# Kernel optimization log

Measured on AMD Instinct MI355X. Metric: run time of the kernel, lower is better.

The kernel has to match this reference:

```python
import jax, jax.numpy as jnp
import numpy as np


def _skip_plan(T, skip_size):
    """Static per-step plan replicating Python list indexing h_i_skips[i - skip_size].

    Returns (slots, use_zero): slot k means 'use h from k+1 steps ago' in the
    rolling buffer (buf[0] == h_{i-1}); use_zero==1 means the skip input is a
    zero init vector.
    """
    slots = np.zeros(T, np.int32)
    use_zero = np.zeros(T, np.float32)
    for i in range(T):
        if i < skip_size:
            # negative Python index: element 2*i of [skip_size zeros] + appended h's
            if 2 * i < skip_size:
                use_zero[i] = 1.0
            else:
                # h_j with j = 2*i - skip_size  ->  lag = i - j = skip_size - i
                slots[i] = (skip_size - i) - 1
        else:
            if i - skip_size < skip_size:
                use_zero[i] = 1.0  # one of the zero inits
            else:
                slots[i] = 2 * skip_size - 1  # h_{i - 2*skip_size}
    return jnp.asarray(slots), jnp.asarray(use_zero)


def setup_inputs() -> dict:
    key = jax.random.key(0)
    ks = jax.random.split(key, 7)
    B, T, X, H = 64, 512, 256, 1024
    s = 1.0 / float(np.sqrt(H))  # PyTorch GRUCell init scale
    x = jax.random.normal(ks[0], (B, T, X), jnp.float32)
    W_ih = jax.random.uniform(ks[1], (3 * H, X), jnp.float32, -s, s)
    W_hh = jax.random.uniform(ks[2], (3 * H, H), jnp.float32, -s, s)
    b_ih = jax.random.uniform(ks[3], (3 * H,), jnp.float32, -s, s)
    b_hh = jax.random.uniform(ks[4], (3 * H,), jnp.float32, -s, s)
    w1 = jax.random.randint(ks[5], (T,), 0, 2, jnp.int32)
    w2_rand = jax.random.randint(ks[6], (T,), 0, 2, jnp.int32)
    w2 = jnp.where(w1 == 0, 1, w2_rand)  # original: W_2 = 1 if W_1 == 0
    return {"x": x, "W_ih": W_ih, "W_hh": W_hh, "b_ih": b_ih, "b_hh": b_hh,
            "w1": w1, "w2": w2, "skip_size": 5}


def reference(x, W_ih, W_hh, b_ih, b_hh, w1, w2, skip_size):
    B, T, X = x.shape
    H = W_hh.shape[1]
    slots, use_zero = _skip_plan(T, int(skip_size))
    # Batch all input projections up-front: [T, B, 3H]
    xi = jnp.einsum('btx,gx->tbg', x, W_ih) + b_ih
    L = 2 * int(skip_size)
    buf0 = jnp.zeros((L, B, H), x.dtype)  # buf[k] = h_{i-1-k}
    w1f = w1.astype(x.dtype)
    w2f = w2.astype(x.dtype)

    def step(buf, xs):
        xi_t, a, b, slot, uz = xs
        h_orig = buf[0]
        h_skip = jax.lax.dynamic_index_in_dim(buf, slot, 0, keepdims=False)
        h = h_orig * a + h_skip * b * (1.0 - uz)
        hh = h @ W_hh.T + b_hh
        xr, xz, xn = jnp.split(xi_t, 3, axis=-1)
        hr, hz, hn = jnp.split(hh, 3, axis=-1)
        r = jax.nn.sigmoid(xr + hr)
        z = jax.nn.sigmoid(xz + hz)
        n = jnp.tanh(xn + r * hn)
        h_new = (1.0 - z) * n + z * h
        buf = jnp.concatenate([h_new[None], buf[:-1]], axis=0)
        return buf, None

    buf, _ = jax.lax.scan(step, buf0, (xi, w1f, w2f, slots, use_zero))
    # h_i_original + h_i_skip, and chunk(repeat) makes them identical
    return 2.0 * buf[0]
```

## Files before the change

kernel.cpp:

```cpp
#include <hip/hip_runtime.h>
#include <hip/hip_bf16.h>
#include <type_traits>

typedef short bf16x8 __attribute__((ext_vector_type(8)));
typedef short bf16x4 __attribute__((ext_vector_type(4)));
typedef float f32x4  __attribute__((ext_vector_type(4)));
typedef int   i32x4  __attribute__((ext_vector_type(4)));
typedef unsigned long long u64;

#define B_   64
#define T_   512
#define XD_  256
#define H_   1024
#define NWG  256
#define NTH  512

#define OFF_WCAT  0UL
#define SZ_WCAT   (3072UL*1280*2)
#define OFF_XB    (OFF_WCAT + SZ_WCAT)
#define SZ_XB     ((unsigned long)T_*B_*XD_*2)
#define OFF_HBF16 (OFF_XB + SZ_XB)
#define SZ_HBF16  (2UL*B_*H_*2)
#define OFF_PLAN  (OFF_HBF16 + SZ_HBF16)
#define SZ_PLAN   (4096UL)
#define OFF_CNT   (OFF_PLAN + SZ_PLAN)
#define SZ_CNT    (8192UL)

__device__ __forceinline__ float sigm_(float x) { return 1.f / (1.f + __expf(-x)); }
__device__ __forceinline__ float tanh_(float x) { return 1.f - 2.f / (__expf(2.f * x) + 1.f); }
__device__ __forceinline__ short bf16_of(float f) {
    __hip_bfloat16 h = __float2bfloat16(f);
    return *reinterpret_cast<short*>(&h);
}
__device__ __forceinline__ float f_of_bf16(short s) {
    union { unsigned u; float f; } c;
    c.u = ((unsigned)(unsigned short)s) << 16;
    return c.f;
}

__global__ void prep_wcat(const float* __restrict__ W_ih, const float* __restrict__ W_hh,
                          short* __restrict__ Wcat) {
    const int j = blockIdx.x;
    for (int k = threadIdx.x; k < 1280; k += 256) {
        float v = (k < XD_) ? W_ih[j * XD_ + k] : W_hh[j * H_ + (k - XD_)];
        Wcat[(long)j * 1280 + k] = bf16_of(v);
    }
}

__global__ void prep_xb(const float* __restrict__ x, short* __restrict__ xb) {
    const long total = (long)T_ * B_ * XD_;
    for (long i = (long)blockIdx.x * blockDim.x + threadIdx.x; i < total;
         i += (long)gridDim.x * blockDim.x) {
        int t   = (int)(i >> 14);
        int rem = (int)(i & 16383);
        int b   = rem >> 8;
        int k   = rem & 255;
        xb[i] = bf16_of(x[((long)(b * T_ + t)) * XD_ + k]);
    }
}

__global__ void prep_plan(const int* __restrict__ w1, const int* __restrict__ w2,
                          const int* __restrict__ ssp, int* __restrict__ plang) {
    int t = threadIdx.x;
    if (t > T_) return;
    if (t == T_) { plang[t] = (1 << 2); return; }
    int ss = ssp[0];
    int a = w1[t] & 1;
    int uz = 0, slot = 0;
    if (t < ss)            { if (2 * t < ss) uz = 1; else slot = ss - t - 1; }
    else if (t - ss < ss)  { uz = 1; }
    else                   { slot = 2 * ss - 1; }
    int bet = uz ? 0 : (w2[t] & 1);
    plang[t] = a | (bet << 1) | ((slot + 1) << 2);
}

__global__ void prep_zero(short* __restrict__ hbf16, int* __restrict__ cnt) {
    int i = blockIdx.x * blockDim.x + threadIdx.x;
    if (i < B_ * H_) hbf16[i] = 0;
    if (i < (int)(SZ_CNT / 4)) cnt[i] = 0;
}

__global__ __launch_bounds__(NTH, 1) void persist_kernel(
    const short* __restrict__ Wcat, const short* __restrict__ xb,
    const float* __restrict__ b_ih, const float* __restrict__ b_hh,
    short* __restrict__ hbf16, const int* __restrict__ plang,
    int* __restrict__ cnt, float* __restrict__ out) {

    __shared__ short Wlds[48 * 1280];
    __shared__ float red[3][7][64][4];
    __shared__ short ringl[16][16][20];
    __shared__ float hbls[2][16][20];
    __shared__ int   planl[T_ + 1];

    const int tid = threadIdx.x;
    const int w   = tid >> 6;
    const int l   = tid & 63;
    const int l15 = l & 15;
    const int lhi = l >> 4;
    const int wg  = blockIdx.x;
    const int c0  = (wg >> 2) << 4;
    const int m0  = (wg & 3) << 4;
    const int dom = wg & 3;
    const int jgr = wg >> 5;
    const int jc0 = c0 + lhi * 4;

    int* lvl1p = cnt + (dom * 8 + jgr) * 32;
    int* rootp = cnt + (32 + dom) * 32;

    for (int j = tid; j < 48 * 160; j += NTH) {
        int r    = j / 160;
        int cbyt = (j - r * 160) * 16;
        int g    = r >> 4, i = r & 15;
        bf16x8 v = *(const bf16x8*)(Wcat + (long)(g * H_ + c0 + i) * 1280 + (cbyt >> 1));
        *(bf16x8*)((char*)Wlds + r * 2560 + (cbyt ^ (i << 4))) = v;
    }
    for (int j = tid; j <= T_; j += NTH) planl[j] = plang[j];
    for (int j = tid; j < 2 * 16 * 20; j += NTH) ((float*)hbls)[j] = 0.f;
    for (int j = tid; j < 16 * 16 * 20; j += NTH) ((short*)ringl)[j] = 0;

    const f32x4 brc = *(const f32x4*)&b_ih[jc0]          + *(const f32x4*)&b_hh[jc0];
    const f32x4 bzc = *(const f32x4*)&b_ih[H_ + jc0]     + *(const f32x4*)&b_hh[H_ + jc0];
    const f32x4 bin = *(const f32x4*)&b_ih[2 * H_ + jc0];
    const f32x4 bhn = *(const f32x4*)&b_hh[2 * H_ + jc0];
    __syncthreads();

    const int swz = l15 << 4;
    auto arow = [&](int g, int kb) -> bf16x8 {
        return *(const bf16x8*)((const char*)Wlds + (g * 16 + l15) * 2560 + (kb ^ swz));
    };

    f32x4 accX[3];
    auto xgemm = [&](int t) {
        accX[0] = accX[1] = accX[2] = (f32x4){0.f, 0.f, 0.f, 0.f};
        const short* xp = xb + ((long)t * B_ + m0 + l15) * XD_ + lhi * 8;
        #pragma unroll
        for (int it = 0; it < 8; ++it) {
            bf16x8 bfrag = *(const bf16x8*)(xp + it * 32);
            const int kb = (it * 32 + lhi * 8) * 2;
            accX[0] = __builtin_amdgcn_mfma_f32_16x16x32_bf16(arow(0, kb), bfrag, accX[0], 0, 0, 0);
            accX[1] = __builtin_amdgcn_mfma_f32_16x16x32_bf16(arow(1, kb), bfrag, accX[1], 0, 0, 0);
            accX[2] = __builtin_amdgcn_mfma_f32_16x16x32_bf16(arow(2, kb), bfrag, accX[2], 0, 0, 0);
        }
    };
    if (w == 0) xgemm(0);

    for (int t = 0; t < T_; ++t) {
        const int par = t & 1;

        if (w == 1 && t > 0) {
            const int tgt = 8 * t;
            const int* rp = rootp;
            while (true) {
                int v;
                asm volatile("global_load_dword %0, %1, off sc0 sc1\n\t"
                             "s_waitcnt vmcnt(0)"
                             : "=&v"(v) : "v"(rp) : "memory");
                if (v >= tgt) break;
                __builtin_amdgcn_s_sleep(1);
            }
        }
        __syncthreads();

        if (w > 0) {
            f32x4 accH[3] = {{0.f,0.f,0.f,0.f},{0.f,0.f,0.f,0.f},{0.f,0.f,0.f,0.f}};
            if (t > 0) {
                auto hgemm = [&](auto ITC, int hk0) {
                    constexpr int IT = decltype(ITC)::value;
                    const short* hp = hbf16 + (long)par * (B_ * H_) + (m0 + l15) * H_ + hk0 + lhi * 8;
                    i32x4 hv[IT];
                    #pragma unroll
                    for (int it = 0; it < IT; ++it)
                        asm volatile("global_load_dwordx4 %0, %1, off sc0 sc1"
                                     : "=&v"(hv[it]) : "v"(hp + it * 32));
                    asm volatile("s_waitcnt vmcnt(0)" ::: "memory");
                    __builtin_amdgcn_sched_barrier(0);
                    #pragma unroll
                    for (int it = 0; it < IT; ++it) {
                        union { i32x4 q; bf16x8 v; } uu; uu.q = hv[it];
                        const int kb = (256 + hk0 + it * 32 + lhi * 8) * 2;
                        accH[0] = __builtin_amdgcn_mfma_f32_16x16x32_bf16(arow(0, kb), uu.v, accH[0], 0, 0, 0);
                        accH[1] = __builtin_amdgcn_mfma_f32_16x16x32_bf16(arow(1, kb), uu.v, accH[1], 0, 0, 0);
                        accH[2] = __builtin_amdgcn_mfma_f32_16x16x32_bf16(arow(2, kb), uu.v, accH[2], 0, 0, 0);
                    }
                };
                if      (w == 1) hgemm(std::integral_constant<int, 5>{}, 0);
                else if (w == 2) hgemm(std::integral_constant<int, 5>{}, 160);
                else if (w == 3) hgemm(std::integral_constant<int, 5>{}, 320);
                else if (w == 4) hgemm(std::integral_constant<int, 5>{}, 480);
                else if (w == 5) hgemm(std::integral_constant<int, 4>{}, 640);
                else if (w == 6) hgemm(std::integral_constant<int, 4>{}, 768);
                else             hgemm(std::integral_constant<int, 4>{}, 896);
            }
            #pragma unroll
            for (int g = 0; g < 3; ++g)
                *(f32x4*)&red[g][w - 1][l][0] = accH[g];
        }
        __syncthreads();

        if (w == 0) {
            f32x4 Hr = {0.f,0.f,0.f,0.f}, Hz = {0.f,0.f,0.f,0.f}, Hn = {0.f,0.f,0.f,0.f};
            #pragma unroll
            for (int s = 0; s < 7; ++s) {
                Hr += *(const f32x4*)&red[0][s][l][0];
                Hz += *(const f32x4*)&red[1][s][l][0];
                Hn += *(const f32x4*)&red[2][s][l][0];
            }
            const int   p   = planl[t + 1];
            const float al  = (float)(p & 1);
            const float bet = (float)((p >> 1) & 1);
            const int   lg  = p >> 2;

            const f32x4 hb = *(const f32x4*)&hbls[par][l15][lhi * 4];
            f32x4 hn;
            #pragma unroll
            for (int r = 0; r < 4; ++r) {
                float rg = sigm_(accX[0][r] + Hr[r] + brc[r]);
                float zg = sigm_(accX[1][r] + Hz[r] + bzc[r]);
                float ng = tanh_(accX[2][r] + bin[r] + rg * (Hn[r] + bhn[r]));
                hn[r] = (1.f - zg) * ng + zg * hb[r];
            }
            union { short s[4]; u64 q; } pk;
            #pragma unroll
            for (int r = 0; r < 4; ++r) pk.s[r] = bf16_of(hn[r]);
            *(bf16x4*)&ringl[t & 15][l15][lhi * 4] = *(bf16x4*)pk.s;
            const bf16x4 old4 = *(const bf16x4*)&ringl[(t + 1 - lg) & 15][l15][lhi * 4];
            f32x4 hbn;
            #pragma unroll
            for (int r = 0; r < 4; ++r)
                hbn[r] = al * hn[r] + bet * f_of_bf16(old4[r]);
            *(f32x4*)&hbls[par ^ 1][l15][lhi * 4] = hbn;

            if (t == T_ - 1) {
                f32x4 o;
                #pragma unroll
                for (int r = 0; r < 4; ++r) o[r] = 2.f * hn[r];
                float* op = out + (long)(m0 + l15) * H_ + jc0;
                asm volatile("global_store_dwordx4 %0, %1, off sc0 sc1"
                             :: "v"(op), "v"(o) : "memory");
            } else {
                #pragma unroll
                for (int r = 0; r < 4; ++r) pk.s[r] = bf16_of(hbn[r]);
                short* pub = hbf16 + (long)(par ^ 1) * (B_ * H_) + (m0 + l15) * H_ + jc0;
                asm volatile("global_store_dwordx2 %0, %1, off sc0 sc1"
                             :: "v"(pub), "v"(pk.q) : "memory");
                asm volatile("s_waitcnt vmcnt(0)" ::: "memory");
                if (l == 0) {
                    int old = __hip_atomic_fetch_add(lvl1p, 1, __ATOMIC_RELAXED,
                                                     __HIP_MEMORY_SCOPE_AGENT);
                    if (old == 8 * (t + 1) - 1)
                        __hip_atomic_fetch_add(rootp, 1, __ATOMIC_RELAXED,
                                               __HIP_MEMORY_SCOPE_AGENT);
                }
                xgemm(t + 1);
            }
        }
    }
}

extern "C" void kernel_launch(void* const* d_in, const int* in_sizes, int n_in,
                              void* d_out, int out_size, void* d_ws, size_t ws_size,
                              hipStream_t stream) {
    const float* x    = (const float*)d_in[0];
    const float* W_ih = (const float*)d_in[1];
    const float* W_hh = (const float*)d_in[2];
    const float* b_ih = (const float*)d_in[3];
    const float* b_hh = (const float*)d_in[4];
    const int*   w1   = (const int*)d_in[5];
    const int*   w2   = (const int*)d_in[6];
    const int*   ssp  = (const int*)d_in[7];
    float* out = (float*)d_out;

    char* ws = (char*)d_ws;
    short* Wcat  = (short*)(ws + OFF_WCAT);
    short* xbuf  = (short*)(ws + OFF_XB);
    short* hbf16 = (short*)(ws + OFF_HBF16);
    int*   plang = (int*)(ws + OFF_PLAN);
    int*   cnt   = (int*)(ws + OFF_CNT);

    prep_wcat<<<3072, 256, 0, stream>>>(W_ih, W_hh, Wcat);
    prep_xb<<<8192, 256, 0, stream>>>(x, xbuf);
    prep_plan<<<1, 1024, 0, stream>>>(w1, w2, ssp, plang);
    prep_zero<<<256, 256, 0, stream>>>(hbf16, cnt);

    persist_kernel<<<NWG, NTH, 0, stream>>>(Wcat, xbuf, b_ih, b_hh,
                                            hbf16, plang, cnt, out);
}
```

Measured before the change: 2.380 ms.

## Replace global root barrier with per-wave waits on needed column-group counters

```diff
diff --git a/kernel.cpp b/kernel.cpp
--- a/kernel.cpp
+++ b/kernel.cpp
@@ -105,7 +105,6 @@
     const int jc0 = c0 + lhi * 4;
 
     int* lvl1p = cnt + (dom * 8 + jgr) * 32;
-    int* rootp = cnt + (32 + dom) * 32;
 
     for (int j = tid; j < 48 * 160; j += NTH) {
         int r    = j / 160;
@@ -147,25 +146,31 @@
     for (int t = 0; t < T_; ++t) {
         const int par = t & 1;
 
-        if (w == 1 && t > 0) {
-            const int tgt = 8 * t;
-            const int* rp = rootp;
-            while (true) {
-                int v;
-                asm volatile("global_load_dword %0, %1, off sc0 sc1\n\t"
-                             "s_waitcnt vmcnt(0)"
-                             : "=&v"(v) : "v"(rp) : "memory");
-                if (v >= tgt) break;
-                __builtin_amdgcn_s_sleep(1);
-            }
-        }
-        __syncthreads();
-
         if (w > 0) {
             f32x4 accH[3] = {{0.f,0.f,0.f,0.f},{0.f,0.f,0.f,0.f},{0.f,0.f,0.f,0.f}};
             if (t > 0) {
                 auto hgemm = [&](auto ITC, int hk0) {
                     constexpr int IT = decltype(ITC)::value;
+                    const int g0 = hk0 >> 7;
+                    const int g1 = (hk0 + IT * 32 - 1) >> 7;
+                    const int* p0 = cnt + (dom * 8 + g0) * 32;
+                    const int* p1 = cnt + (dom * 8 + g1) * 32;
+                    const int* p2 = lvl1p;
+                    const int  tgt = 8 * t;
+                    while (true) {
+                        int v0, v1, v2;
+                        asm volatile("global_load_dword %0, %3, off sc0 sc1\n\t"
+                                     "global_load_dword %1, %4, off sc0 sc1\n\t"
+                                     "global_load_dword %2, %5, off sc0 sc1\n\t"
+                                     "s_waitcnt vmcnt(0)"
+                                     : "=&v"(v0), "=&v"(v1), "=&v"(v2)
+                                     : "v"(p0), "v"(p1), "v"(p2) : "memory");
+                        int mn = v0 < v1 ? v0 : v1;
+                        mn = mn < v2 ? mn : v2;
+                        if (mn >= tgt) break;
+                        __builtin_amdgcn_s_sleep(1);
+                    }
+                    __builtin_amdgcn_sched_barrier(0);
                     const short* hp = hbf16 + (long)par * (B_ * H_) + (m0 + l15) * H_ + hk0 + lhi * 8;
                     i32x4 hv[IT];
                     #pragma unroll
@@ -244,13 +249,9 @@
                 asm volatile("global_store_dwordx2 %0, %1, off sc0 sc1"
                              :: "v"(pub), "v"(pk.q) : "memory");
                 asm volatile("s_waitcnt vmcnt(0)" ::: "memory");
-                if (l == 0) {
-                    int old = __hip_atomic_fetch_add(lvl1p, 1, __ATOMIC_RELAXED,
-                                                     __HIP_MEMORY_SCOPE_AGENT);
-                    if (old == 8 * (t + 1) - 1)
-                        __hip_atomic_fetch_add(rootp, 1, __ATOMIC_RELAXED,
-                                               __HIP_MEMORY_SCOPE_AGENT);
-                }
+                if (l == 0)
+                    __hip_atomic_fetch_add(lvl1p, 1, __ATOMIC_RELAXED,
+                                           __HIP_MEMORY_SCOPE_AGENT);
                 xgemm(t + 1);
             }
         }
```

Measured after the change: 2.521 ms. 1.06x slower.

## Spread GRU gate epilogue across all eight waves with LDS counter before publish

Applied to the files above, without the earlier changes.

```diff
diff --git a/kernel.cpp b/kernel.cpp
--- a/kernel.cpp
+++ b/kernel.cpp
@@ -87,10 +87,11 @@
     int* __restrict__ cnt, float* __restrict__ out) {
 
     __shared__ short Wlds[48 * 1280];
-    __shared__ float red[3][7][64][4];
+    __shared__ float red[3][8][64][4];
     __shared__ short ringl[16][16][20];
     __shared__ float hbls[2][16][20];
-    __shared__ int   planl[T_ + 1];
+    __shared__ int   planl[T_ + 4];
+    __shared__ int   acnt;
 
     const int tid = threadIdx.x;
     const int w   = tid >> 6;
@@ -102,7 +103,6 @@
     const int m0  = (wg & 3) << 4;
     const int dom = wg & 3;
     const int jgr = wg >> 5;
-    const int jc0 = c0 + lhi * 4;
 
     int* lvl1p = cnt + (dom * 8 + jgr) * 32;
     int* rootp = cnt + (32 + dom) * 32;
@@ -117,11 +117,16 @@
     for (int j = tid; j <= T_; j += NTH) planl[j] = plang[j];
     for (int j = tid; j < 2 * 16 * 20; j += NTH) ((float*)hbls)[j] = 0.f;
     for (int j = tid; j < 16 * 16 * 20; j += NTH) ((short*)ringl)[j] = 0;
-
-    const f32x4 brc = *(const f32x4*)&b_ih[jc0]          + *(const f32x4*)&b_hh[jc0];
-    const f32x4 bzc = *(const f32x4*)&b_ih[H_ + jc0]     + *(const f32x4*)&b_hh[H_ + jc0];
-    const f32x4 bin = *(const f32x4*)&b_ih[2 * H_ + jc0];
-    const f32x4 bhn = *(const f32x4*)&b_hh[2 * H_ + jc0];
+    if (tid == 0) acnt = 0;
+
+    const int  bt   = (w << 1) | (l >> 2);
+    const int  cq   = (l & 3) << 2;
+    const int  idx4 = ((l & 3) << 4) + ((w << 1) | (l >> 2));
+    const int  jc   = c0 + cq;
+    const f32x4 br_e  = *(const f32x4*)&b_ih[jc]          + *(const f32x4*)&b_hh[jc];
+    const f32x4 bz_e  = *(const f32x4*)&b_ih[H_ + jc]     + *(const f32x4*)&b_hh[H_ + jc];
+    const f32x4 bin_e = *(const f32x4*)&b_ih[2 * H_ + jc];
+    const f32x4 bhn_e = *(const f32x4*)&b_hh[2 * H_ + jc];
     __syncthreads();
 
     const int swz = l15 << 4;
@@ -161,7 +166,11 @@
         }
         __syncthreads();
 
-        if (w > 0) {
+        if (w == 0) {
+            #pragma unroll
+            for (int g = 0; g < 3; ++g)
+                *(f32x4*)&red[g][7][l][0] = accX[g];
+        } else {
             f32x4 accH[3] = {{0.f,0.f,0.f,0.f},{0.f,0.f,0.f,0.f},{0.f,0.f,0.f,0.f}};
             if (t > 0) {
                 auto hgemm = [&](auto ITC, int hk0) {
@@ -197,63 +206,76 @@
         }
         __syncthreads();
 
-        if (w == 0) {
-            f32x4 Hr = {0.f,0.f,0.f,0.f}, Hz = {0.f,0.f,0.f,0.f}, Hn = {0.f,0.f,0.f,0.f};
-            #pragma unroll
-            for (int s = 0; s < 7; ++s) {
-                Hr += *(const f32x4*)&red[0][s][l][0];
-                Hz += *(const f32x4*)&red[1][s][l][0];
-                Hn += *(const f32x4*)&red[2][s][l][0];
-            }
+        {
             const int   p   = planl[t + 1];
             const float al  = (float)(p & 1);
             const float bet = (float)((p >> 1) & 1);
             const int   lg  = p >> 2;
 
-            const f32x4 hb = *(const f32x4*)&hbls[par][l15][lhi * 4];
-            f32x4 hn;
-            #pragma unroll
-            for (int r = 0; r < 4; ++r) {
-                float rg = sigm_(accX[0][r] + Hr[r] + brc[r]);
-                float zg = sigm_(accX[1][r] + Hz[r] + bzc[r]);
-                float ng = tanh_(accX[2][r] + bin[r] + rg * (Hn[r] + bhn[r]));
-                hn[r] = (1.f - zg) * ng + zg * hb[r];
+            if (l < 8) {
+                f32x4 Hr = {0,0,0,0}, Hz = {0,0,0,0}, Hn = {0,0,0,0};
+                #pragma unroll
+                for (int s = 0; s < 8; ++s) {
+                    Hr += *(const f32x4*)&red[0][s][idx4][0];
+                    Hz += *(const f32x4*)&red[1][s][idx4][0];
+                }
+                #pragma unroll
+                for (int s = 0; s < 7; ++s)
+                    Hn += *(const f32x4*)&red[2][s][idx4][0];
+                const f32x4 Xn = *(const f32x4*)&red[2][7][idx4][0];
+
+                const f32x4 hb = *(const f32x4*)&hbls[par][bt][cq];
+                f32x4 hn;
+                #pragma unroll
+                for (int r = 0; r < 4; ++r) {
+                    float rg = sigm_(Hr[r] + br_e[r]);
+                    float zg = sigm_(Hz[r] + bz_e[r]);
+                    float ng = tanh_(Xn[r] + bin_e[r] + rg * (Hn[r] + bhn_e[r]));
+                    hn[r] = (1.f - zg) * ng + zg * hb[r];
+                }
+                union { short s[4]; u64 q; } pk;
+                #pragma unroll
+                for (int r = 0; r < 4; ++r) pk.s[r] = bf16_of(hn[r]);
+                *(bf16x4*)&ringl[t & 15][bt][cq] = *(bf16x4*)pk.s;
+                const bf16x4 old4 = *(const bf16x4*)&ringl[(t + 1 - lg) & 15][bt][cq];
+                f32x4 hbn;
+                #pragma unroll
+                for (int r = 0; r < 4; ++r)
+                    hbn[r] = al * hn[r] + bet * f_of_bf16(old4[r]);
+                *(f32x4*)&hbls[par ^ 1][bt][cq] = hbn;
+
+                if (t == T_ - 1) {
+                    f32x4 o;
+                    #pragma unroll
+                    for (int r = 0; r < 4; ++r) o[r] = 2.f * hn[r];
+                    float* op = out + (long)(m0 + bt) * H_ + jc;
+                    asm volatile("global_store_dwordx4 %0, %1, off sc0 sc1"
+                                 :: "v"(op), "v"(o) : "memory");
+                } else {
+                    #pragma unroll
+                    for (int r = 0; r < 4; ++r) pk.s[r] = bf16_of(hbn[r]);
+                    short* pub = hbf16 + (long)(par ^ 1) * (B_ * H_) + (m0 + bt) * H_ + jc;
+                    asm volatile("global_store_dwordx2 %0, %1, off sc0 sc1"
+                                 :: "v"(pub), "v"(pk.q) : "memory");
+                }
             }
-            union { short s[4]; u64 q; } pk;
-            #pragma unroll
-            for (int r = 0; r < 4; ++r) pk.s[r] = bf16_of(hn[r]);
-            *(bf16x4*)&ringl[t & 15][l15][lhi * 4] = *(bf16x4*)pk.s;
-            const bf16x4 old4 = *(const bf16x4*)&ringl[(t + 1 - lg) & 15][l15][lhi * 4];
-            f32x4 hbn;
-            #pragma unroll
-            for (int r = 0; r < 4; ++r)
-                hbn[r] = al * hn[r] + bet * f_of_bf16(old4[r]);
-            *(f32x4*)&hbls[par ^ 1][l15][lhi * 4] = hbn;
-
-            if (t == T_ - 1) {
-                f32x4 o;
-                #pragma unroll
-                for (int r = 0; r < 4; ++r) o[r] = 2.f * hn[r];
-                float* op = out + (long)(m0 + l15) * H_ + jc0;
-                asm volatile("global_store_dwordx4 %0, %1, off sc0 sc1"
-                             :: "v"(op), "v"(o) : "memory");
-            } else {
-                #pragma unroll
-                for (int r = 0; r < 4; ++r) pk.s[r] = bf16_of(hbn[r]);
-                short* pub = hbf16 + (long)(par ^ 1) * (B_ * H_) + (m0 + l15) * H_ + jc0;
-                asm volatile("global_store_dwordx2 %0, %1, off sc0 sc1"
-                             :: "v"(pub), "v"(pk.q) : "memory");
+
+            if (t < T_ - 1) {
                 asm volatile("s_waitcnt vmcnt(0)" ::: "memory");
                 if (l == 0) {
-                    int old = __hip_atomic_fetch_add(lvl1p, 1, __ATOMIC_RELAXED,
-                                                     __HIP_MEMORY_SCOPE_AGENT);
-                    if (old == 8 * (t + 1) - 1)
-                        __hip_atomic_fetch_add(rootp, 1, __ATOMIC_RELAXED,
-                                               __HIP_MEMORY_SCOPE_AGENT);
+                    int oldl = atomicAdd(&acnt, 1);
+                    if (oldl == 8 * (t + 1) - 1) {
+                        int old = __hip_atomic_fetch_add(lvl1p, 1, __ATOMIC_RELAXED,
+                                                         __HIP_MEMORY_SCOPE_AGENT);
+                        if (old == 8 * (t + 1) - 1)
+                            __hip_atomic_fetch_add(rootp, 1, __ATOMIC_RELAXED,
+                                                   __HIP_MEMORY_SCOPE_AGENT);
+                    }
                 }
-                xgemm(t + 1);
             }
         }
+
+        if (w == 0 && t + 1 < T_) xgemm(t + 1);
     }
 }
 
```

Measured after the change: 3.040 ms. 27.7% more time.

## Replace hierarchical atomic counter barrier with per-workgroup flag polling

Applied to the files above, without the earlier changes.

```diff
diff --git a/kernel.cpp b/kernel.cpp
--- a/kernel.cpp
+++ b/kernel.cpp
@@ -23,8 +23,8 @@
 #define SZ_HBF16  (2UL*B_*H_*2)
 #define OFF_PLAN  (OFF_HBF16 + SZ_HBF16)
 #define SZ_PLAN   (4096UL)
-#define OFF_CNT   (OFF_PLAN + SZ_PLAN)
-#define SZ_CNT    (8192UL)
+#define OFF_FLAG  (OFF_PLAN + SZ_PLAN)
+#define SZ_FLAG   (4096UL)
 
 __device__ __forceinline__ float sigm_(float x) { return 1.f / (1.f + __expf(-x)); }
 __device__ __forceinline__ float tanh_(float x) { return 1.f - 2.f / (__expf(2.f * x) + 1.f); }
@@ -74,17 +74,21 @@
     plang[t] = a | (bet << 1) | ((slot + 1) << 2);
 }
 
-__global__ void prep_zero(short* __restrict__ hbf16, int* __restrict__ cnt) {
+__global__ void prep_zero(short* __restrict__ hbf16, int* __restrict__ flags) {
     int i = blockIdx.x * blockDim.x + threadIdx.x;
     if (i < B_ * H_) hbf16[i] = 0;
-    if (i < (int)(SZ_CNT / 4)) cnt[i] = 0;
+    if (i < 1024) {
+        int* p = flags + i;
+        int z = 0;
+        asm volatile("global_store_dword %0, %1, off sc0 sc1" :: "v"(p), "v"(z) : "memory");
+    }
 }
 
 __global__ __launch_bounds__(NTH, 1) void persist_kernel(
     const short* __restrict__ Wcat, const short* __restrict__ xb,
     const float* __restrict__ b_ih, const float* __restrict__ b_hh,
     short* __restrict__ hbf16, const int* __restrict__ plang,
-    int* __restrict__ cnt, float* __restrict__ out) {
+    int* __restrict__ flags, float* __restrict__ out) {
 
     __shared__ short Wlds[48 * 1280];
     __shared__ float red[3][7][64][4];
@@ -101,11 +105,8 @@
     const int c0  = (wg >> 2) << 4;
     const int m0  = (wg & 3) << 4;
     const int dom = wg & 3;
-    const int jgr = wg >> 5;
+    const int cblk = wg >> 2;
     const int jc0 = c0 + lhi * 4;
-
-    int* lvl1p = cnt + (dom * 8 + jgr) * 32;
-    int* rootp = cnt + (32 + dom) * 32;
 
     for (int j = tid; j < 48 * 160; j += NTH) {
         int r    = j / 160;
@@ -148,15 +149,17 @@
         const int par = t & 1;
 
         if (w == 1 && t > 0) {
-            const int tgt = 8 * t;
-            const int* rp = rootp;
+            const int* fa = flags + dom * 64 + l15 * 4;
             while (true) {
-                int v;
-                asm volatile("global_load_dword %0, %1, off sc0 sc1\n\t"
+                i32x4 f;
+                asm volatile("global_load_dwordx4 %0, %1, off sc0 sc1\n\t"
                              "s_waitcnt vmcnt(0)"
-                             : "=&v"(v) : "v"(rp) : "memory");
-                if (v >= tgt) break;
-                __builtin_amdgcn_s_sleep(1);
+                             : "=&v"(f) : "v"(fa) : "memory");
+                int m01 = f[0] < f[1] ? f[0] : f[1];
+                int m23 = f[2] < f[3] ? f[2] : f[3];
+                int mn  = m01 < m23 ? m01 : m23;
+                if (__all((l < 16) ? (mn >= t) : 1)) break;
+                __builtin_amdgcn_s_sleep(2);
             }
         }
         __syncthreads();
@@ -245,11 +248,10 @@
                              :: "v"(pub), "v"(pk.q) : "memory");
                 asm volatile("s_waitcnt vmcnt(0)" ::: "memory");
                 if (l == 0) {
-                    int old = __hip_atomic_fetch_add(lvl1p, 1, __ATOMIC_RELAXED,
-                                                     __HIP_MEMORY_SCOPE_AGENT);
-                    if (old == 8 * (t + 1) - 1)
-                        __hip_atomic_fetch_add(rootp, 1, __ATOMIC_RELAXED,
-                                               __HIP_MEMORY_SCOPE_AGENT);
+                    int  fv = t + 1;
+                    int* fp = flags + dom * 64 + cblk;
+                    asm volatile("global_store_dword %0, %1, off sc0 sc1"
+                                 :: "v"(fp), "v"(fv) : "memory");
                 }
                 xgemm(t + 1);
             }
@@ -275,13 +277,13 @@
     short* xbuf  = (short*)(ws + OFF_XB);
     short* hbf16 = (short*)(ws + OFF_HBF16);
     int*   plang = (int*)(ws + OFF_PLAN);
-    int*   cnt   = (int*)(ws + OFF_CNT);
+    int*   flags = (int*)(ws + OFF_FLAG);
 
     prep_wcat<<<3072, 256, 0, stream>>>(W_ih, W_hh, Wcat);
     prep_xb<<<8192, 256, 0, stream>>>(x, xbuf);
     prep_plan<<<1, 1024, 0, stream>>>(w1, w2, ssp, plang);
-    prep_zero<<<256, 256, 0, stream>>>(hbf16, cnt);
+    prep_zero<<<256, 256, 0, stream>>>(hbf16, flags);
 
     persist_kernel<<<NWG, NTH, 0, stream>>>(Wcat, xbuf, b_ih, b_hh,
-                                            hbf16, plang, cnt, out);
-}
+                                            hbf16, plang, flags, out);
+}
```

After: 2.193 ms. -7.8%, faster.
